# Optimization experiments

Hardware: AMD Instinct MI355X
Metric: run time of the kernel (lower is better)

Reference implementation:

```python
import jax, jax.numpy as jnp
import numpy as np

# dims
L, B, S, D, H, DH, DF = 4, 4, 1024, 1024, 16, 64, 4096  # layers, batch, seq, d_model, heads, head_dim, ffn
EPS = 1e-5


def setup_inputs() -> dict:
    key = jax.random.key(0)
    ks = jax.random.split(key, 22)
    sD = 1.0 / np.sqrt(D)
    sF = 1.0 / np.sqrt(DF)
    sR = 1.0 / np.sqrt(DH)  # W_r init: normal(std=1/sqrt(d_r))
    inp = {
        'src': jax.random.normal(ks[0], (B, S, D), jnp.float32),
        'src_mask': jnp.ones((B, 1, 1, S), jnp.int32),
        'ln1_g': jnp.ones((L, D)), 'ln1_b': jnp.zeros((L, D)),
        'Wq': jax.random.normal(ks[1], (L, D, H * DH)) * sD,
        'bq': jnp.zeros((L, H * DH)),
        'Wk': jax.random.normal(ks[2], (L, D, H * DH)) * sD,
        'bk': jnp.zeros((L, H * DH)),
        'Wv': jax.random.normal(ks[3], (L, D, H * DH)) * sD,
        'bv': jnp.zeros((L, H * DH)),
        'Wr': jax.random.normal(ks[4], (L, D, H * DH)) * sR,
        'br': jnp.zeros((L, H * DH)),
        'Wo': jax.random.normal(ks[5], (L, H * DH, D)) * sD,
        'bo': jnp.zeros((L, D)),
        'ln2_g': jnp.ones((L, D)), 'ln2_b': jnp.zeros((L, D)),
        'W1': jax.random.normal(ks[6], (L, D, DF)) * sD,
        'b1': jnp.zeros((L, DF)),
        'W2': jax.random.normal(ks[7], (L, DF, D)) * sF,
        'b2': jnp.zeros((L, D)),
        'ln3_g': jnp.ones((L, D)), 'ln3_b': jnp.zeros((L, D)),
    }
    return inp


def _ln(x, g, b):
    m = x.mean(-1, keepdims=True)
    v = ((x - m) ** 2).mean(-1, keepdims=True)
    return (x - m) * jax.lax.rsqrt(v + EPS) * g + b


def _encoder(src, src_mask, params):
    scale = 1.0 / np.sqrt(DH)  # 1/sqrt(d_k)

    def layer(x, p):
        (l1g, l1b, wq, bq, wk, bk, wv, bv, wr, br, wo, bo,
         l2g, l2b, w1, b1, w2, b2, l3g, l3b) = p
        z = _ln(x, l1g, l1b)
        # projections -> [B, S, H, DH] ('bihd' layout)
        Q = (z @ wq + bq).reshape(B, S, H, DH)
        K = (z @ wk + bk).reshape(B, S, H, DH)
        V = (z @ wv + bv).reshape(B, S, H, DH)
        R = (z @ wr + br).reshape(B, S, H, DH)
        dot = jnp.einsum('bihd,bjhd->bhij', Q, K) * scale
        dot = jnp.where(src_mask == 0, -1e10, dot)  # mask [B,1,1,S] broadcasts
        attn = jax.nn.softmax(dot, axis=-1)
        v_bar = jnp.einsum('bjhd,bhij->bihd', V, attn)
        new_v = v_bar * R  # elementwise role gate
        out = new_v.reshape(B, S, H * DH) @ wo + bo
        mha_res = x + out
        z2 = _ln(mha_res, l2g, l2b)
        ff = jax.nn.relu(z2 @ w1 + b1) @ w2 + b2
        return _ln(mha_res + ff, l3g, l3b), None

    out, _ = jax.lax.scan(layer, src, params)
    return out


def reference(src, src_mask, ln1_g, ln1_b, Wq, bq, Wk, bk, Wv, bv, Wr, br,
              Wo, bo, ln2_g, ln2_b, W1, b1, W2, b2, ln3_g, ln3_b):
    params = (ln1_g, ln1_b, Wq, bq, Wk, bk, Wv, bv, Wr, br, Wo, bo,
              ln2_g, ln2_b, W1, b1, W2, b2, ln3_g, ln3_b)
    return _encoder(src, src_mask, params)
```

## Files before the change

### kernel.cpp

```cpp
#include <hip/hip_runtime.h>


typedef _Float16 f16;
typedef _Float16 f16x8 __attribute__((ext_vector_type(8)));
typedef _Float16 f16x4 __attribute__((ext_vector_type(4)));
typedef float    f32x4 __attribute__((ext_vector_type(4)));

#define GPTR(x) (const __attribute__((address_space(1))) void*)(x)
#define LPTR(x) (__attribute__((address_space(3))) void*)(x)
#define MFMA16(a,b,c) __builtin_amdgcn_mfma_f32_16x16x32_f16(a, b, c, 0, 0, 0)

static constexpr int NB   = 4;
static constexpr int NS   = 1024;
static constexpr int ND   = 1024;
static constexpr int NH   = 16;
static constexpr int NDH  = 64;
static constexpr int NDF  = 4096;
static constexpr int NM   = NB * NS;
static constexpr int HD   = NH * NDH;
static constexpr float kC1 = 0.180336879f;

#define EPI_H      0
#define EPI_VT     1
#define EPI_RELU   2
#define EPI_RESF32 3
#define EPI_QKVR   4

__global__ __launch_bounds__(256) void transpose_cvt(
    const float* __restrict__ src, f16* __restrict__ dst,
    int R, int C, int srcZ, int dstZ)
{
  src += (size_t)blockIdx.z * srcZ;
  dst += (size_t)blockIdx.z * dstZ;
  __shared__ float tile[64][65];
  int t  = threadIdx.x;
  int c0 = blockIdx.x * 64, r0 = blockIdx.y * 64;
  int tr = t >> 4, tc4 = (t & 15) * 4;
#pragma unroll
  for (int i = 0; i < 4; ++i) {
    float4 v = *(const float4*)&src[(size_t)(r0 + tr + i * 16) * C + c0 + tc4];
    tile[tr + i * 16][tc4 + 0] = v.x;
    tile[tr + i * 16][tc4 + 1] = v.y;
    tile[tr + i * 16][tc4 + 2] = v.z;
    tile[tr + i * 16][tc4 + 3] = v.w;
  }
  __syncthreads();
  int n = t >> 2, ks = (t & 3) * 16;
  f16x8 o0, o1;
#pragma unroll
  for (int j = 0; j < 8; ++j) {
    o0[j] = (f16)tile[ks + j][n];
    o1[j] = (f16)tile[ks + 8 + j][n];
  }
  f16* dp = &dst[(size_t)(c0 + n) * R + r0 + ks];
  *(f16x8*)dp       = o0;
  *(f16x8*)(dp + 8) = o1;
}

__global__ __launch_bounds__(256) void pack_bias(
    const float* __restrict__ bq, const float* __restrict__ bk,
    const float* __restrict__ bv, const float* __restrict__ br,
    const float* __restrict__ bo, const float* __restrict__ b1,
    const float* __restrict__ b2, float* __restrict__ dst)
{
  int i = blockIdx.x * 256 + threadIdx.x;
  if (i >= 4 * 10240) return;
  int l = i / 10240, o = i % 10240;
  float v;
  if      (o < 1024) v = bq[l * 1024 + o];
  else if (o < 2048) v = bk[l * 1024 + o - 1024];
  else if (o < 3072) v = bv[l * 1024 + o - 2048];
  else if (o < 4096) v = br[l * 1024 + o - 3072];
  else if (o < 5120) v = bo[l * 1024 + o - 4096];
  else if (o < 9216) v = b1[l * 4096 + o - 5120];
  else               v = b2[l * 1024 + o - 9216];
  dst[i] = v;
}

template<bool F16OUT>
__global__ __launch_bounds__(256) void ln_kernel(
    const float* __restrict__ in, const float* __restrict__ g,
    const float* __restrict__ b, void* __restrict__ out)
{
  int row = blockIdx.x, t = threadIdx.x;
  float4 v = *(const float4*)&in[(size_t)row * ND + t * 4];
  float s  = v.x + v.y + v.z + v.w;
  float sq = v.x * v.x + v.y * v.y + v.z * v.z + v.w * v.w;
#pragma unroll
  for (int off = 32; off; off >>= 1) {
    s  += __shfl_xor(s, off, 64);
    sq += __shfl_xor(sq, off, 64);
  }
  __shared__ float rb[8];
  int wid = t >> 6;
  if ((t & 63) == 0) { rb[wid] = s; rb[4 + wid] = sq; }
  __syncthreads();
  s  = rb[0] + rb[1] + rb[2] + rb[3];
  sq = rb[4] + rb[5] + rb[6] + rb[7];
  float mean = s * (1.0f / ND);
  float var  = sq * (1.0f / ND) - mean * mean;
  float rstd = rsqrtf(var + 1e-5f);
  float4 g4 = *(const float4*)&g[t * 4];
  float4 b4 = *(const float4*)&b[t * 4];
  float o0 = (v.x - mean) * rstd * g4.x + b4.x;
  float o1 = (v.y - mean) * rstd * g4.y + b4.y;
  float o2 = (v.z - mean) * rstd * g4.z + b4.z;
  float o3 = (v.w - mean) * rstd * g4.w + b4.w;
  if (F16OUT) {
    f16x4 ov = { (f16)o0, (f16)o1, (f16)o2, (f16)o3 };
    *(f16x4*)((f16*)out + (size_t)row * ND + t * 4) = ov;
  } else {
    float4 ov = { o0, o1, o2, o3 };
    *(float4*)((float*)out + (size_t)row * ND + t * 4) = ov;
  }
}

template<int EPIMODE>
__global__ __launch_bounds__(512, 2) void gemm256(
    const f16* __restrict__ A, const f16* __restrict__ Bt,
    const float* __restrict__ bias, f16* __restrict__ outH, int K)
{
  constexpr int BM = 256, BN = 256, BK = 64;
  constexpr int ASZ = BM * BK;
  constexpr int TSZ = 2 * ASZ;
  __shared__ f16 sm[2 * TSZ];

  int lin = blockIdx.x + (blockIdx.y << 4);
  int l2  = (lin & 7) * 32 + (lin >> 3);
  int by  = l2 & 15, bx = l2 >> 4;

  int t = threadIdx.x;
  int wid = t >> 6, lane = t & 63;
  int wr = wid >> 2, wc = wid & 3;
  int rA = lane & 15, kg = lane >> 4;
  int m0 = bx * BM, n0 = by * BN;

  f32x4 acc[8][4] = {};
  const f16* Abase = A  + (size_t)m0 * K;
  const f16* Bbase = Bt + (size_t)n0 * K;

  auto stage = [&](int buf, int kt) {
    f16* As = sm + buf * TSZ;
    f16* Bs = As + ASZ;
#pragma unroll
    for (int i = 0; i < 4; ++i) {
      int p = i * 512 + t;
      int row = p >> 3, c = (p & 7) ^ (row & 7);
      __builtin_amdgcn_global_load_lds(
          GPTR(Abase + (size_t)row * K + kt + c * 8),
          LPTR(As + (i * 512 + wid * 64) * 8), 16, 0, 0);
    }
#pragma unroll
    for (int i = 0; i < 4; ++i) {
      int p = i * 512 + t;
      int row = p >> 3, c = (p & 7) ^ (row & 7);
      __builtin_amdgcn_global_load_lds(
          GPTR(Bbase + (size_t)row * K + kt + c * 8),
          LPTR(Bs + (i * 512 + wid * 64) * 8), 16, 0, 0);
    }
  };

  int nIt = K / BK;
  stage(0, 0);
  stage(1, BK);
  for (int it = 0; it < nIt; ++it) {
    int cur = it & 1;
    if (it + 1 < nIt) {
      asm volatile("s_waitcnt vmcnt(8)" ::: "memory");
    } else {
      asm volatile("s_waitcnt vmcnt(0)" ::: "memory");
    }
    __builtin_amdgcn_s_barrier();
    __builtin_amdgcn_sched_barrier(0);
    const f16* As = sm + cur * TSZ;
    const f16* Bs = As + ASZ;
#pragma unroll
    for (int h = 0; h < 2; ++h) {
      f16x8 af[8], bf[4];
#pragma unroll
      for (int m = 0; m < 8; ++m) {
        int r = wr * 128 + m * 16 + rA;
        af[m] = *(const f16x8*)&As[r * BK + (((h * 4 + kg) ^ (r & 7)) * 8)];
      }
#pragma unroll
      for (int n = 0; n < 4; ++n) {
        int r = wc * 64 + n * 16 + rA;
        bf[n] = *(const f16x8*)&Bs[r * BK + (((h * 4 + kg) ^ (r & 7)) * 8)];
      }
#pragma unroll
      for (int m = 0; m < 8; ++m)
#pragma unroll
        for (int n = 0; n < 4; ++n)
          acc[m][n] = MFMA16(af[m], bf[n], acc[m][n]);
    }
    if (it + 2 < nIt) {
      __builtin_amdgcn_sched_barrier(0);
      __builtin_amdgcn_s_barrier();
      stage(cur, (it + 2) * BK);
    }
  }

  __builtin_amdgcn_sched_barrier(0);
  __builtin_amdgcn_s_barrier();
  if (EPIMODE == EPI_QKVR && (n0 >> 10) == 2) {
    f16* vt = outH + (size_t)2 * 4194304;
#pragma unroll
    for (int n = 0; n < 4; ++n) {
      int gn = n0 + wc * 64 + n * 16 + rA;
      int gnl = gn & 1023;
      float bvv = bias[gn];
#pragma unroll
      for (int m = 0; m < 8; ++m) {
        int gmb = m0 + wr * 128 + m * 16 + kg * 4;
        f16x4 ov = { (f16)(acc[m][n][0] + bvv), (f16)(acc[m][n][1] + bvv),
                     (f16)(acc[m][n][2] + bvv), (f16)(acc[m][n][3] + bvv) };
        *(f16x4*)&vt[(size_t)gnl * NM + gmb] = ov;
      }
    }
  } else {
    bool scaleQ = (EPIMODE == EPI_QKVR) && ((n0 >> 10) == 0);
#pragma unroll
    for (int n = 0; n < 4; ++n) {
      int cl = wc * 64 + n * 16 + rA;
      float bvv = bias[n0 + cl];
#pragma unroll
      for (int m = 0; m < 8; ++m) {
        int rl = wr * 128 + m * 16 + kg * 4;
#pragma unroll
        for (int r = 0; r < 4; ++r) {
          float v = acc[m][n][r] + bvv;
          if (EPIMODE == EPI_RELU) v = fmaxf(v, 0.0f);
          if (scaleQ) v *= kC1;
          sm[(rl + r) * 256 + cl] = (f16)v;
        }
      }
    }
    __syncthreads();
    f16* outp;
    int ldo, col0;
    if (EPIMODE == EPI_QKVR) {
      int z = n0 >> 10;
      outp = outH + (size_t)z * 4194304; ldo = 1024; col0 = n0 & 1023;
    } else {
      outp = outH; ldo = 4096; col0 = n0;
    }
#pragma unroll
    for (int i = 0; i < 16; ++i) {
      int p = i * 512 + t;
      int row = p >> 5, c8 = p & 31;
      *(f16x8*)&outp[(size_t)(m0 + row) * ldo + col0 + c8 * 8] =
          *(const f16x8*)&sm[row * 256 + c8 * 8];
    }
  }
}

template<int BM, int BN, int BK>
__global__ __launch_bounds__(256) void gemm_bt(
    const f16* __restrict__ A, const f16* __restrict__ Bt,
    const float* __restrict__ bias, const float* __restrict__ res,
    f16* __restrict__ outH, float* __restrict__ outF,
    int N, int K, int epi, int zBt, int zBias, int zOut)
{
  constexpr int CH = BK / 8;
  constexpr int CM = CH - 1;
  constexpr int KH = BK / 32;
  constexpr int FM = BM / 32, FN = BN / 32;
  constexpr int ASZ = BM * BK, BSZ = BN * BK;
  constexpr int TSZ = ASZ + BSZ;
  constexpr int LPT = (BM + BN) * CH / 256;
  constexpr int SMEM = (3 * TSZ > BM * BN) ? 3 * TSZ : BM * BN;
  __shared__ f16 sm[SMEM];

  auto SWZ = [](int row) { return ((CH == 4) ? (row >> 1) : row) & CM; };

  int nx = gridDim.x, ny = gridDim.y;
  int lin = blockIdx.x + nx * (blockIdx.y + ny * blockIdx.z);
  int tot = nx * ny * gridDim.z;
  int l2  = (lin & 7) * (tot >> 3) + (lin >> 3);
  int by  = l2 % ny; int rem = l2 / ny; int bx = rem % nx; int z = rem / nx;

  Bt += (size_t)z * zBt;
  const float* biasz = bias + (size_t)z * zBias;
  int ep = (epi == EPI_QKVR) ? ((z == 2) ? EPI_VT : EPI_H) : epi;

  int t = threadIdx.x;
  int wid = t >> 6, lane = t & 63;
  int wr = wid >> 1, wc = wid & 1;
  int rA = lane & 15, kg = lane >> 4;
  int m0 = bx * BM, n0 = by * BN;

  f32x4 acc[FM][FN] = {};
  const f16* Abase = A  + (size_t)m0 * K;
  const f16* Bbase = Bt + (size_t)n0 * K;

  auto stage = [&](int buf, int kt) {
    f16* As = sm + buf * TSZ;
    f16* Bs = As + ASZ;
#pragma unroll
    for (int i = 0; i < BM * CH / 256; ++i) {
      int p = i * 256 + t;
      int row = p / CH, c = (p & CM) ^ SWZ(row);
      __builtin_amdgcn_global_load_lds(
          GPTR(Abase + (size_t)row * K + kt + c * 8),
          LPTR(As + (i * 256 + wid * 64) * 8), 16, 0, 0);
    }
#pragma unroll
    for (int i = 0; i < BN * CH / 256; ++i) {
      int p = i * 256 + t;
      int row = p / CH, c = (p & CM) ^ SWZ(row);
      __builtin_amdgcn_global_load_lds(
          GPTR(Bbase + (size_t)row * K + kt + c * 8),
          LPTR(Bs + (i * 256 + wid * 64) * 8), 16, 0, 0);
    }
  };

  int nIt = K / BK;
  stage(0, 0);
  if (nIt > 1) stage(1, BK);
  int cur = 0, nxt = 2;
  for (int it = 0; it < nIt; ++it) {
    if (it + 1 < nIt) {
      asm volatile("s_waitcnt vmcnt(%0)" :: "n"(LPT) : "memory");
    } else {
      asm volatile("s_waitcnt vmcnt(0)" ::: "memory");
    }
    __builtin_amdgcn_s_barrier();
    __builtin_amdgcn_sched_barrier(0);
    if (it + 2 < nIt) stage(nxt, (it + 2) * BK);
    const f16* As = sm + cur * TSZ;
    const f16* Bs = As + ASZ;
    f16x8 af[FM][KH], bf[FN][KH];
#pragma unroll
    for (int m = 0; m < FM; ++m) {
      int r = wr * (BM / 2) + m * 16 + rA;
#pragma unroll
      for (int h = 0; h < KH; ++h)
        af[m][h] = *(const f16x8*)&As[r * BK + (((h * 4 + kg) ^ SWZ(r)) * 8)];
    }
#pragma unroll
    for (int n = 0; n < FN; ++n) {
      int r = wc * (BN / 2) + n * 16 + rA;
#pragma unroll
      for (int h = 0; h < KH; ++h)
        bf[n][h] = *(const f16x8*)&Bs[r * BK + (((h * 4 + kg) ^ SWZ(r)) * 8)];
    }
#pragma unroll
    for (int h = 0; h < KH; ++h)
#pragma unroll
      for (int m = 0; m < FM; ++m)
#pragma unroll
        for (int n = 0; n < FN; ++n)
          acc[m][n] = MFMA16(af[m][h], bf[n][h], acc[m][n]);
    cur = (cur == 2) ? 0 : cur + 1;
    nxt = (nxt == 2) ? 0 : nxt + 1;
  }

  if (ep == EPI_H || ep == EPI_RELU) {
    __builtin_amdgcn_s_barrier();
#pragma unroll
    for (int n = 0; n < FN; ++n) {
      int cl = wc * (BN / 2) + n * 16 + rA;
      float bvv = biasz[n0 + cl];
#pragma unroll
      for (int m = 0; m < FM; ++m) {
        int rl = wr * (BM / 2) + m * 16 + kg * 4;
#pragma unroll
        for (int r = 0; r < 4; ++r) {
          float v = acc[m][n][r] + bvv;
          if (ep == EPI_RELU) v = fmaxf(v, 0.0f);
          sm[(rl + r) * BN + cl] = (f16)v;
        }
      }
    }
    __syncthreads();
    f16* outp = outH + (size_t)z * zOut;
#pragma unroll
    for (int i = 0; i < BM * BN / 2048; ++i) {
      int p = i * 256 + t;
      int row = p / (BN / 8), c8 = p % (BN / 8);
      *(f16x8*)&outp[(size_t)(m0 + row) * N + n0 + c8 * 8] =
          *(const f16x8*)&sm[row * BN + c8 * 8];
    }
  } else {
#pragma unroll
    for (int n = 0; n < FN; ++n) {
      int gn = n0 + wc * (BN / 2) + n * 16 + rA;
      float bvv = biasz[gn];
#pragma unroll
      for (int m = 0; m < FM; ++m) {
        int gmb = m0 + wr * (BM / 2) + m * 16 + kg * 4;
        if (ep == EPI_VT) {
          f16x4 ov = { (f16)(acc[m][n][0] + bvv), (f16)(acc[m][n][1] + bvv),
                       (f16)(acc[m][n][2] + bvv), (f16)(acc[m][n][3] + bvv) };
          *(f16x4*)&outH[(size_t)z * zOut + (size_t)gn * NM + gmb] = ov;
        } else {
#pragma unroll
          for (int r = 0; r < 4; ++r) {
            int gm = gmb + r;
            outF[(size_t)gm * N + gn] =
                acc[m][n][r] + bvv + res[(size_t)gm * N + gn];
          }
        }
      }
    }
  }
}

__global__ __launch_bounds__(256) void attn_kernel(
    const f16* __restrict__ Qm, const f16* __restrict__ Km,
    const f16* __restrict__ Vt, const f16* __restrict__ Rm,
    f16* __restrict__ outA)
{
  int t = threadIdx.x, wid = t >> 6, lane = t & 63;
  int rA = lane & 15, kg = lane >> 4;
  int id = blockIdx.x;
  int j = id >> 3;
  int bh = (id & 7) * 8 + (j & 7), qb = j >> 3;
  int b = bh >> 4, h = bh & 15;
  int q0 = qb * 128 + wid * 32;

  __shared__ f16 KVs[2][2 * 64 * 64];
  __shared__ f16 P[4][32 * 64];
  f16* Pw = P[wid];

  f16x8 aq[2][2];
#pragma unroll
  for (int mf = 0; mf < 2; ++mf) {
    size_t qoff = (size_t)(b * NS + q0 + mf * 16 + rA) * HD + h * NDH + kg * 8;
    aq[mf][0] = *(const f16x8*)&Qm[qoff];
    aq[mf][1] = *(const f16x8*)&Qm[qoff + 32];
  }

  f32x4 o[2][4] = {};
  f32x4 osum[2] = {};
  f16x8 vones;
#pragma unroll
  for (int jj = 0; jj < 8; ++jj) vones[jj] = (f16)1.0f;

  auto stage = [&](int buf, int kv) {
    f16* Ks = KVs[buf];
    f16* Vs = Ks + 64 * 64;
#pragma unroll
    for (int i = 0; i < 2; ++i) {
      int p = i * 256 + t;
      int row = p >> 3, c16 = (p & 7) ^ (row & 7);
      __builtin_amdgcn_global_load_lds(
          GPTR(Km + (size_t)(b * NS + kv + row) * HD + h * NDH + c16 * 8),
          LPTR(Ks + (i * 256 + wid * 64) * 8), 16, 0, 0);
    }
#pragma unroll
    for (int i = 0; i < 2; ++i) {
      int p = i * 256 + t;
      int row = p >> 3, c16 = (p & 7) ^ (row & 7);
      __builtin_amdgcn_global_load_lds(
          GPTR(Vt + (size_t)(h * NDH + row) * NM + b * NS + kv + c16 * 8),
          LPTR(Vs + (i * 256 + wid * 64) * 8), 16, 0, 0);
    }
  };

  stage(0, 0);
  stage(1, 64);
  for (int tt = 0; tt < NS / 64; ++tt) {
    int cur = tt & 1;
    if (tt + 1 < NS / 64) {
      asm volatile("s_waitcnt vmcnt(4)" ::: "memory");
    } else {
      asm volatile("s_waitcnt vmcnt(0)" ::: "memory");
    }
    __builtin_amdgcn_s_barrier();
    __builtin_amdgcn_sched_barrier(0);
    const f16* Kc = KVs[cur];
    const f16* Vc = Kc + 64 * 64;

    f32x4 sc[2][4];
#pragma unroll
    for (int ct = 0; ct < 4; ++ct) {
      int krow = ct * 16 + rA;
      f16x8 kb0 = *(const f16x8*)&Kc[krow * 64 + ((kg ^ (rA & 7)) * 8)];
      f16x8 kb1 = *(const f16x8*)&Kc[krow * 64 + (((4 + kg) ^ (rA & 7)) * 8)];
#pragma unroll
      for (int mf = 0; mf < 2; ++mf) {
        f32x4 a = {};
        a = MFMA16(aq[mf][0], kb0, a);
        a = MFMA16(aq[mf][1], kb1, a);
        sc[mf][ct] = a;
      }
    }

#pragma unroll
    for (int mf = 0; mf < 2; ++mf)
#pragma unroll
      for (int ct = 0; ct < 4; ++ct)
#pragma unroll
        for (int r = 0; r < 4; ++r) {
          float arg = fminf(sc[mf][ct][r], 14.5f);
          float p;
          asm("v_exp_f32 %0, %1" : "=v"(p) : "v"(arg));
          Pw[(mf * 16 + kg * 4 + r) * 64 + ((ct ^ kg) * 16 + rA)] = (f16)p;
        }

#pragma unroll
    for (int kc = 0; kc < 2; ++kc) {
      f16x8 vb[4];
#pragma unroll
      for (int dt = 0; dt < 4; ++dt)
        vb[dt] = *(const f16x8*)&Vc[(dt * 16 + rA) * 64 + (((kc * 4 + kg) ^ (rA & 7)) * 8)];
#pragma unroll
      for (int mf = 0; mf < 2; ++mf) {
        f16x8 pa = *(const f16x8*)&Pw[(mf * 16 + rA) * 64 + ((kc * 32 + kg * 8) ^ ((rA >> 2) << 4))];
#pragma unroll
        for (int dt = 0; dt < 4; ++dt)
          o[mf][dt] = MFMA16(pa, vb[dt], o[mf][dt]);
        osum[mf] = MFMA16(pa, vones, osum[mf]);
      }
    }
    if (tt + 2 < NS / 64) {
      __builtin_amdgcn_sched_barrier(0);
      __builtin_amdgcn_s_barrier();
      stage(cur, (tt + 2) * 64);
    }
  }

  float lrinv[2][4];
#pragma unroll
  for (int mf = 0; mf < 2; ++mf)
#pragma unroll
    for (int r = 0; r < 4; ++r) lrinv[mf][r] = 1.0f / osum[mf][r];
#pragma unroll
  for (int mf = 0; mf < 2; ++mf)
#pragma unroll
    for (int dt = 0; dt < 4; ++dt)
#pragma unroll
      for (int r = 0; r < 4; ++r) {
        size_t idx = (size_t)(b * NS + q0 + mf * 16 + kg * 4 + r) * HD + h * NDH + dt * 16 + rA;
        float v = o[mf][dt][r] * lrinv[mf][r] * (float)Rm[idx];
        outA[idx] = (f16)v;
      }
}

extern "C" void kernel_launch(void* const* d_in, const int* in_sizes, int n_in,
                              void* d_out, int out_size, void* d_ws, size_t ws_size,
                              hipStream_t stream)
{
  const float* src  = (const float*)d_in[0];
  const float* ln1g = (const float*)d_in[2];
  const float* ln1b = (const float*)d_in[3];
  const float* Wq   = (const float*)d_in[4];
  const float* bq   = (const float*)d_in[5];
  const float* Wk   = (const float*)d_in[6];
  const float* bk   = (const float*)d_in[7];
  const float* Wv   = (const float*)d_in[8];
  const float* bv   = (const float*)d_in[9];
  const float* Wr   = (const float*)d_in[10];
  const float* br   = (const float*)d_in[11];
  const float* Wo   = (const float*)d_in[12];
  const float* bo   = (const float*)d_in[13];
  const float* ln2g = (const float*)d_in[14];
  const float* ln2b = (const float*)d_in[15];
  const float* W1   = (const float*)d_in[16];
  const float* b1   = (const float*)d_in[17];
  const float* W2   = (const float*)d_in[18];
  const float* b2   = (const float*)d_in[19];
  const float* ln3g = (const float*)d_in[20];
  const float* ln3b = (const float*)d_in[21];

  char* ws = (char*)d_ws;
  float* biasbuf = (float*)ws;
  size_t off = 40960 * sizeof(float);
  const size_t WT_L = 13631488;
  size_t act_bytes = (size_t)NM * 1024 * 20;
  bool upfront = ws_size >= off + 4 * WT_L * 2 + act_bytes;
  f16* wt = (f16*)(ws + off);
  off += (upfront ? 4 : 1) * WT_L * 2;
  float* xbuf = (float*)(ws + off); off += (size_t)NM * ND * 4;
  float* mha  = (float*)(ws + off); off += (size_t)NM * ND * 4;
  f16* zbuf   = (f16*)(ws + off);   off += (size_t)NM * ND * 2;
  f16* qkvr   = (f16*)(ws + off);   off += (size_t)NM * ND * 2 * 4;
  f16* aout   = (f16*)(ws + off);

  pack_bias<<<160, 256, 0, stream>>>(bq, bk, bv, br, bo, b1, b2, biasbuf);

  if (upfront) {
    transpose_cvt<<<dim3(16, 16, 4), 256, 0, stream>>>(Wq, wt + 0,       1024, 1024, 1048576, (int)WT_L);
    transpose_cvt<<<dim3(16, 16, 4), 256, 0, stream>>>(Wk, wt + 1048576, 1024, 1024, 1048576, (int)WT_L);
    transpose_cvt<<<dim3(16, 16, 4), 256, 0, stream>>>(Wv, wt + 2097152, 1024, 1024, 1048576, (int)WT_L);
    transpose_cvt<<<dim3(16, 16, 4), 256, 0, stream>>>(Wr, wt + 3145728, 1024, 1024, 1048576, (int)WT_L);
    transpose_cvt<<<dim3(16, 16, 4), 256, 0, stream>>>(Wo, wt + 4194304, 1024, 1024, 1048576, (int)WT_L);
    transpose_cvt<<<dim3(64, 16, 4), 256, 0, stream>>>(W1, wt + 5242880, 1024, 4096, 4194304, (int)WT_L);
    transpose_cvt<<<dim3(16, 64, 4), 256, 0, stream>>>(W2, wt + 9437184, 4096, 1024, 4194304, (int)WT_L);
  }

  for (int l = 0; l < 4; ++l) {
    f16* wtL = upfront ? wt + (size_t)l * WT_L : wt;
    const float* bL = biasbuf + l * 10240;
    if (!upfront) {
      transpose_cvt<<<dim3(16, 16, 1), 256, 0, stream>>>(Wq + (size_t)l * 1048576, wt + 0,       1024, 1024, 0, 0);
      transpose_cvt<<<dim3(16, 16, 1), 256, 0, stream>>>(Wk + (size_t)l * 1048576, wt + 1048576, 1024, 1024, 0, 0);
      transpose_cvt<<<dim3(16, 16, 1), 256, 0, stream>>>(Wv + (size_t)l * 1048576, wt + 2097152, 1024, 1024, 0, 0);
      transpose_cvt<<<dim3(16, 16, 1), 256, 0, stream>>>(Wr + (size_t)l * 1048576, wt + 3145728, 1024, 1024, 0, 0);
      transpose_cvt<<<dim3(16, 16, 1), 256, 0, stream>>>(Wo + (size_t)l * 1048576, wt + 4194304, 1024, 1024, 0, 0);
      transpose_cvt<<<dim3(64, 16, 1), 256, 0, stream>>>(W1 + (size_t)l * 4194304, wt + 5242880, 1024, 4096, 0, 0);
      transpose_cvt<<<dim3(16, 64, 1), 256, 0, stream>>>(W2 + (size_t)l * 4194304, wt + 9437184, 4096, 1024, 0, 0);
    }
    const float* xin = l ? xbuf : src;

    ln_kernel<true><<<NM, 256, 0, stream>>>(xin, ln1g + l * 1024, ln1b + l * 1024, zbuf);
    gemm256<EPI_QKVR><<<dim3(16, 16), 512, 0, stream>>>(zbuf, wtL, bL, qkvr, 1024);
    attn_kernel<<<dim3(512), 256, 0, stream>>>(
        qkvr, qkvr + 4194304, qkvr + 8388608, qkvr + 12582912, aout);
    gemm_bt<128, 64, 64><<<dim3(32, 16, 1), 256, 0, stream>>>(
        aout, wtL + 4194304, bL + 4096, xin, nullptr, mha, 1024, 1024, EPI_RESF32, 0, 0, 0);
    ln_kernel<true><<<NM, 256, 0, stream>>>(mha, ln2g + l * 1024, ln2b + l * 1024, zbuf);
    gemm256<EPI_RELU><<<dim3(16, 16), 512, 0, stream>>>(zbuf, wtL + 5242880, bL + 5120, qkvr, 1024);
    gemm_bt<128, 64, 64><<<dim3(32, 16, 1), 256, 0, stream>>>(
        qkvr, wtL + 9437184, bL + 9216, mha, nullptr, mha, 1024, 4096, EPI_RESF32, 0, 0, 0);
    float* lnout = (l == 3) ? (float*)d_out : xbuf;
    ln_kernel<false><<<NM, 256, 0, stream>>>(mha, ln3g + l * 1024, ln3b + l * 1024, lnout);
  }
}
```

Measured before the change: 857.2 us.

## Split GEMM inner loop into quadrant phases with early stage issue and setprio

Restructures the main GEMM k-loop into four quadrant phases: LDS fragment loads for a sub-block are followed by a waitcnt and a burst of MFMAs at raised wave priority, with barriers between phases. The next tile's global-to-LDS stage is issued before the last quadrant's MFMAs, so it overlaps compute instead of waiting for the whole tile. This targets the LDS-load and MFMA serialization and the memory stall at the end of each iteration. The cost is more barriers per iteration and higher register pressure, since both k-halves of the fragments stay live.

```diff
diff --git a/kernel.cpp b/kernel.cpp
--- a/kernel.cpp
+++ b/kernel.cpp
@@ -174,33 +174,91 @@
     __builtin_amdgcn_sched_barrier(0);
     const f16* As = sm + cur * TSZ;
     const f16* Bs = As + ASZ;
-#pragma unroll
-    for (int h = 0; h < 2; ++h) {
-      f16x8 af[8], bf[4];
-#pragma unroll
-      for (int m = 0; m < 8; ++m) {
-        int r = wr * 128 + m * 16 + rA;
-        af[m] = *(const f16x8*)&As[r * BK + (((h * 4 + kg) ^ (r & 7)) * 8)];
-      }
-#pragma unroll
-      for (int n = 0; n < 4; ++n) {
-        int r = wc * 64 + n * 16 + rA;
-        bf[n] = *(const f16x8*)&Bs[r * BK + (((h * 4 + kg) ^ (r & 7)) * 8)];
-      }
-#pragma unroll
-      for (int m = 0; m < 8; ++m)
-#pragma unroll
-        for (int n = 0; n < 4; ++n)
-          acc[m][n] = MFMA16(af[m], bf[n], acc[m][n]);
-    }
-    if (it + 2 < nIt) {
-      __builtin_amdgcn_sched_barrier(0);
-      __builtin_amdgcn_s_barrier();
-      stage(cur, (it + 2) * BK);
-    }
-  }
-
-  __builtin_amdgcn_sched_barrier(0);
+    f16x8 af[8][2], bf[4][2];
+
+#pragma unroll
+    for (int m = 0; m < 4; ++m) {
+      int r = wr * 128 + m * 16 + rA;
+#pragma unroll
+      for (int h = 0; h < 2; ++h)
+        af[m][h] = *(const f16x8*)&As[r * BK + (((h * 4 + kg) ^ (r & 7)) * 8)];
+    }
+#pragma unroll
+    for (int n = 0; n < 2; ++n) {
+      int r = wc * 64 + n * 16 + rA;
+#pragma unroll
+      for (int h = 0; h < 2; ++h)
+        bf[n][h] = *(const f16x8*)&Bs[r * BK + (((h * 4 + kg) ^ (r & 7)) * 8)];
+    }
+    asm volatile("s_waitcnt lgkmcnt(0)" ::: "memory");
+    __builtin_amdgcn_sched_barrier(0);
+    __builtin_amdgcn_s_setprio(1);
+#pragma unroll
+    for (int h = 0; h < 2; ++h)
+#pragma unroll
+      for (int m = 0; m < 4; ++m)
+#pragma unroll
+        for (int n = 0; n < 2; ++n)
+          acc[m][n] = MFMA16(af[m][h], bf[n][h], acc[m][n]);
+    __builtin_amdgcn_s_setprio(0);
+    __builtin_amdgcn_sched_barrier(0);
+    __builtin_amdgcn_s_barrier();
+
+#pragma unroll
+    for (int n = 2; n < 4; ++n) {
+      int r = wc * 64 + n * 16 + rA;
+#pragma unroll
+      for (int h = 0; h < 2; ++h)
+        bf[n][h] = *(const f16x8*)&Bs[r * BK + (((h * 4 + kg) ^ (r & 7)) * 8)];
+    }
+    asm volatile("s_waitcnt lgkmcnt(0)" ::: "memory");
+    __builtin_amdgcn_sched_barrier(0);
+    __builtin_amdgcn_s_setprio(1);
+#pragma unroll
+    for (int h = 0; h < 2; ++h)
+#pragma unroll
+      for (int m = 0; m < 4; ++m)
+#pragma unroll
+        for (int n = 2; n < 4; ++n)
+          acc[m][n] = MFMA16(af[m][h], bf[n][h], acc[m][n]);
+    __builtin_amdgcn_s_setprio(0);
+    __builtin_amdgcn_sched_barrier(0);
+    __builtin_amdgcn_s_barrier();
+
+#pragma unroll
+    for (int m = 4; m < 8; ++m) {
+      int r = wr * 128 + m * 16 + rA;
+#pragma unroll
+      for (int h = 0; h < 2; ++h)
+        af[m][h] = *(const f16x8*)&As[r * BK + (((h * 4 + kg) ^ (r & 7)) * 8)];
+    }
+    asm volatile("s_waitcnt lgkmcnt(0)" ::: "memory");
+    __builtin_amdgcn_sched_barrier(0);
+    __builtin_amdgcn_s_setprio(1);
+#pragma unroll
+    for (int h = 0; h < 2; ++h)
+#pragma unroll
+      for (int m = 4; m < 8; ++m)
+#pragma unroll
+        for (int n = 0; n < 2; ++n)
+          acc[m][n] = MFMA16(af[m][h], bf[n][h], acc[m][n]);
+    __builtin_amdgcn_s_setprio(0);
+    __builtin_amdgcn_sched_barrier(0);
+    __builtin_amdgcn_s_barrier();
+
+    if (it + 2 < nIt) stage(cur, (it + 2) * BK);
+    __builtin_amdgcn_s_setprio(1);
+#pragma unroll
+    for (int h = 0; h < 2; ++h)
+#pragma unroll
+      for (int m = 4; m < 8; ++m)
+#pragma unroll
+        for (int n = 2; n < 4; ++n)
+          acc[m][n] = MFMA16(af[m][h], bf[n][h], acc[m][n]);
+    __builtin_amdgcn_s_setprio(0);
+    __builtin_amdgcn_sched_barrier(0);
+  }
+
   __builtin_amdgcn_s_barrier();
   if (EPIMODE == EPI_QKVR && (n0 >> 10) == 2) {
     f16* vt = outH + (size_t)2 * 4194304;
```

New measurement: 856.3 us (median of 2 runs). No clear change (-0.1%).

## Restructure GEMM mainloop into 8-phase quadrant schedule with staggered half-tile prefetch

Applied to the files above, without the earlier changes.

Replaces the simple double-buffered K loop with a two-tile-per-iteration schedule. Each tile is split into four MFMA quadrants, and each quadrant is interleaved with LDS fragment reads and half-tile global_load_lds prefetches, separated by barriers. MFMA blocks are wrapped in s_setprio to favour matrix issue. The goal is to hide LDS and global load latency behind MFMA work and to reduce register pressure from whole-tile fragment loads, at the cost of many more barriers and a tricky buffer-reuse ordering.

```diff
diff --git a/kernel.cpp b/kernel.cpp
--- a/kernel.cpp
+++ b/kernel.cpp
@@ -9,6 +9,8 @@
 #define GPTR(x) (const __attribute__((address_space(1))) void*)(x)
 #define LPTR(x) (__attribute__((address_space(3))) void*)(x)
 #define MFMA16(a,b,c) __builtin_amdgcn_mfma_f32_16x16x32_f16(a, b, c, 0, 0, 0)
+#define SBAR()  __builtin_amdgcn_s_barrier()
+#define SCHB()  __builtin_amdgcn_sched_barrier(0)
 
 static constexpr int NB   = 4;
 static constexpr int NS   = 1024;
@@ -139,69 +141,126 @@
   const f16* Abase = A  + (size_t)m0 * K;
   const f16* Bbase = Bt + (size_t)n0 * K;
 
-  auto stage = [&](int buf, int kt) {
-    f16* As = sm + buf * TSZ;
-    f16* Bs = As + ASZ;
-#pragma unroll
-    for (int i = 0; i < 4; ++i) {
-      int p = i * 512 + t;
-      int row = p >> 3, c = (p & 7) ^ (row & 7);
+  auto stageHalf = [&](int slot, int isB, int h, int kt) {
+    const f16* g = isB ? Bbase : Abase;
+    f16* dst = sm + slot * TSZ + isB * ASZ;
+#pragma unroll
+    for (int i = 0; i < 2; ++i) {
+      int p  = h * 1024 + i * 512 + t;
+      int rt = p >> 3;
+      int c  = (p & 7) ^ (rt & 7);
       __builtin_amdgcn_global_load_lds(
-          GPTR(Abase + (size_t)row * K + kt + c * 8),
-          LPTR(As + (i * 512 + wid * 64) * 8), 16, 0, 0);
-    }
-#pragma unroll
-    for (int i = 0; i < 4; ++i) {
-      int p = i * 512 + t;
-      int row = p >> 3, c = (p & 7) ^ (row & 7);
-      __builtin_amdgcn_global_load_lds(
-          GPTR(Bbase + (size_t)row * K + kt + c * 8),
-          LPTR(Bs + (i * 512 + wid * 64) * 8), 16, 0, 0);
+          GPTR(g + (size_t)rt * K + kt + c * 8),
+          LPTR(dst + ((h * 1024 + i * 512) + wid * 64) * 8), 16, 0, 0);
     }
   };
 
-  int nIt = K / BK;
-  stage(0, 0);
-  stage(1, BK);
+#define READ_AF(As_, mlo_)                                                   \
+  _Pragma("unroll")                                                          \
+  for (int m = (mlo_); m < (mlo_) + 4; ++m) {                                \
+    int r = wr * 128 + m * 16 + rA;                                          \
+    _Pragma("unroll")                                                        \
+    for (int h = 0; h < 2; ++h)                                              \
+      af[m][h] = *(const f16x8*)&(As_)[r * BK + (((h*4+kg) ^ (r&7)) * 8)];   \
+  }
+#define READ_BF(Bs_, nlo_)                                                   \
+  _Pragma("unroll")                                                          \
+  for (int n = (nlo_); n < (nlo_) + 2; ++n) {                                \
+    int r = wc * 64 + n * 16 + rA;                                           \
+    _Pragma("unroll")                                                        \
+    for (int h = 0; h < 2; ++h)                                              \
+      bf[n][h] = *(const f16x8*)&(Bs_)[r * BK + (((h*4+kg) ^ (r&7)) * 8)];   \
+  }
+#define MFMAQ(mlo_, nlo_)                                                    \
+  __builtin_amdgcn_s_setprio(1);                                             \
+  _Pragma("unroll")                                                          \
+  for (int h = 0; h < 2; ++h)                                                \
+    _Pragma("unroll")                                                        \
+    for (int m = (mlo_); m < (mlo_) + 4; ++m)                                \
+      _Pragma("unroll")                                                      \
+      for (int n = (nlo_); n < (nlo_) + 2; ++n)                              \
+        acc[m][n] = MFMA16(af[m][h], bf[n][h], acc[m][n]);                   \
+  __builtin_amdgcn_s_setprio(0);
+#define PHASE_SYNC_RD()  SCHB(); SBAR();                                     \
+  asm volatile("s_waitcnt lgkmcnt(0)" ::: "memory"); SCHB()
+#define PHASE_END()      SCHB(); SBAR()
+
+  int nIt = K / 128;
+  stageHalf(0, 1, 0, 0);  stageHalf(0, 1, 1, 0);
+  stageHalf(0, 0, 0, 0);  stageHalf(0, 0, 1, 0);
+  stageHalf(1, 1, 0, 64); stageHalf(1, 1, 1, 64);
+
   for (int it = 0; it < nIt; ++it) {
-    int cur = it & 1;
-    if (it + 1 < nIt) {
-      asm volatile("s_waitcnt vmcnt(8)" ::: "memory");
+    int kt1  = it * 128 + 64;
+    int ktn0 = it * 128 + 128;
+    int ktn1 = it * 128 + 192;
+    bool sn = (it + 1 < nIt);
+    const f16* A0s = sm;
+    const f16* B0s = sm + ASZ;
+    const f16* A1s = sm + TSZ;
+    const f16* B1s = sm + TSZ + ASZ;
+    f16x8 af[8][2], bf[4][2];
+
+    asm volatile("s_waitcnt vmcnt(4)" ::: "memory");
+    SCHB(); SBAR(); SCHB();
+    READ_AF(A0s, 0) READ_BF(B0s, 0)
+    stageHalf(1, 0, 0, kt1);
+    PHASE_SYNC_RD();
+    MFMAQ(0, 0)
+    PHASE_END();
+
+    READ_BF(B0s, 2)
+    stageHalf(1, 0, 1, kt1);
+    PHASE_SYNC_RD();
+    MFMAQ(0, 2)
+    PHASE_END();
+
+    READ_AF(A0s, 4)
+    if (sn) stageHalf(0, 1, 0, ktn0);
+    PHASE_SYNC_RD();
+    MFMAQ(4, 0)
+    PHASE_END();
+
+    if (sn) stageHalf(0, 1, 1, ktn0);
+    SCHB(); SBAR();
+    MFMAQ(4, 2)
+    PHASE_END();
+
+    if (sn) {
+      asm volatile("s_waitcnt vmcnt(4)" ::: "memory");
     } else {
       asm volatile("s_waitcnt vmcnt(0)" ::: "memory");
     }
-    __builtin_amdgcn_s_barrier();
-    __builtin_amdgcn_sched_barrier(0);
-    const f16* As = sm + cur * TSZ;
-    const f16* Bs = As + ASZ;
-#pragma unroll
-    for (int h = 0; h < 2; ++h) {
-      f16x8 af[8], bf[4];
-#pragma unroll
-      for (int m = 0; m < 8; ++m) {
-        int r = wr * 128 + m * 16 + rA;
-        af[m] = *(const f16x8*)&As[r * BK + (((h * 4 + kg) ^ (r & 7)) * 8)];
-      }
-#pragma unroll
-      for (int n = 0; n < 4; ++n) {
-        int r = wc * 64 + n * 16 + rA;
-        bf[n] = *(const f16x8*)&Bs[r * BK + (((h * 4 + kg) ^ (r & 7)) * 8)];
-      }
-#pragma unroll
-      for (int m = 0; m < 8; ++m)
-#pragma unroll
-        for (int n = 0; n < 4; ++n)
-          acc[m][n] = MFMA16(af[m], bf[n], acc[m][n]);
-    }
-    if (it + 2 < nIt) {
-      __builtin_amdgcn_sched_barrier(0);
-      __builtin_amdgcn_s_barrier();
-      stage(cur, (it + 2) * BK);
-    }
-  }
-
-  __builtin_amdgcn_sched_barrier(0);
-  __builtin_amdgcn_s_barrier();
+    SCHB(); SBAR(); SCHB();
+    READ_AF(A1s, 0) READ_BF(B1s, 0)
+    if (sn) stageHalf(0, 0, 0, ktn0);
+    PHASE_SYNC_RD();
+    MFMAQ(0, 0)
+    PHASE_END();
+
+    READ_BF(B1s, 2)
+    if (sn) stageHalf(0, 0, 1, ktn0);
+    PHASE_SYNC_RD();
+    MFMAQ(0, 2)
+    PHASE_END();
+
+    READ_AF(A1s, 4)
+    if (sn) stageHalf(1, 1, 0, ktn1);
+    PHASE_SYNC_RD();
+    MFMAQ(4, 0)
+    PHASE_END();
+
+    if (sn) stageHalf(1, 1, 1, ktn1);
+    SCHB(); SBAR();
+    MFMAQ(4, 2)
+    PHASE_END();
+  }
+#undef READ_AF
+#undef READ_BF
+#undef MFMAQ
+#undef PHASE_SYNC_RD
+#undef PHASE_END
+
   if (EPIMODE == EPI_QKVR && (n0 >> 10) == 2) {
     f16* vt = outH + (size_t)2 * 4194304;
 #pragma unroll
```

After: 860.8 us. No clear change (+0.4%).
